# Optimization experiments

Measured on AMD Instinct MI355X. Metric: run time of the kernel, lower is better.

## Reference

```python
import math
import jax, jax.numpy as jnp
import numpy as np

N, C, H, W = 32, 128, 56, 56


def unfold3(x, axis, dil):
    """F.unfold with 3-tap kernel along `axis`, dilation `dil`, padding `dil`.
    Input (n,c,h,w) -> output (n,c,3,h,w); tap k takes offset (k-1)*dil."""
    pad_cfg = [(0, 0)] * 4
    pad_cfg[axis] = (dil, dil)
    xp = jnp.pad(x, pad_cfg)
    size = x.shape[axis]
    taps = [jax.lax.slice_in_dim(xp, k * dil, k * dil + size, axis=axis) for k in range(3)]
    return jnp.stack(taps, axis=2)


def setup_inputs() -> dict:
    key = jax.random.key(0)
    k0, k1, k2, k3, k4 = jax.random.split(key, 5)
    x = jax.random.normal(k0, (N, C, H, W), dtype=jnp.float32)
    # trunc_normal_(std=0.02) approximated by normal * 0.02
    p2 = jax.random.normal(k1, (1, 1, 3, 1, W), dtype=jnp.float32) * 0.02
    # 1x1 conv weight (out=C, in=3C), kaiming-ish scale
    p3 = jax.random.normal(k2, (C, 3 * C), dtype=jnp.float32) * (1.0 / math.sqrt(3 * C))
    p5 = jax.random.normal(k3, (1, 1, H, W), dtype=jnp.float32) * 0.02
    p10 = jax.random.normal(k4, (1, C, 3, H, W), dtype=jnp.float32) * 0.02
    return {"x": x, "p2": p2, "p3": p3, "p5": p5, "p10": p10}


def reference(x, p2, p3, p5, p10):
    n, c, h, w = x.shape
    # t_1: vertical 3-tap unfold, dilation 2 -> (n,c,3,h,w)
    t1 = unfold3(x, axis=2, dil=2)
    t2 = p2 * t1                                              # (n,c,3,h,w)
    # t_3: 1x1 conv over the c*3 channel view
    t3 = jnp.einsum('nkhw,ck->nchw', t1.reshape(n, c * 3, h, w), p3)
    # t_4: horizontal 3-tap unfold, dilation 1
    t4 = unfold3(t3, axis=3, dil=1)                           # (n,c,3,h,w)
    t5 = p5 * t3                                              # (n,c,h,w)
    # t_7/t_8: horizontal 3-tap unfold of x, dilation 2, softmax over taps
    t7 = unfold3(x, axis=3, dil=2)
    t8 = jax.nn.softmax(t7, axis=2)                           # (n,c,3,h,w)
    # t_9: bmm over spatial dim -> (n,c,c*3)
    t9 = jnp.einsum('ncx,ndx->ncd', x.reshape(n, c, h * w),
                    t4.reshape(n, c * 3, h * w)) / math.sqrt(h * w)
    t10 = p10 * t8                                            # (n,c,3,h,w)
    # t_11: memory-reinterpreting view: (n,1,c,h,w) - (n,3,c,h,w) -> back to (n,c,3,h,w)
    t11 = (t5[:, None] - t2.reshape(n, 3, c, h, w)).reshape(n, c, 3, h, w)
    t12 = t11 - t10                                           # (n,c,3,h,w)
    # t_13: bmm over c*3 -> (n,c,h*w)
    t13 = jnp.einsum('ncd,ndx->ncx', t9,
                     t12.reshape(n, c * 3, h * w)) / math.sqrt(c * 3)
    return t13.reshape(n, c, h, w)
```

## Files before the change

kernel.cpp:

```cpp
#include <hip/hip_runtime.h>
#include <stdint.h>

#define NB 32
#define C_ 128
#define H_ 56
#define W_ 56
#define HW 3136
#define KD 384

typedef __attribute__((ext_vector_type(8))) short bf16x8;
typedef __attribute__((ext_vector_type(4))) float f32x4;

__device__ inline uint16_t f2bf(float f) {
    uint32_t u = __float_as_uint(f);
    return (uint16_t)((u + 0x7FFFu + ((u >> 16) & 1u)) >> 16);
}
__device__ inline float bf2f(uint16_t b) {
    return __uint_as_float(((uint32_t)b) << 16);
}

__global__ __launch_bounds__(256) void p1_xtp(const float* __restrict__ x,
                                              uint16_t* __restrict__ xtp,
                                              uint16_t* __restrict__ xb) {
    __shared__ uint16_t lt[56][136];
    const int h = blockIdx.x, n = blockIdx.y, tid = threadIdx.x;
    const int c = tid >> 1, wh = tid & 1;
    const float* xr = &x[(((size_t)n * C_ + c) * H_ + h) * W_ + wh * 28];
    uint32_t pk[14];
#pragma unroll
    for (int q = 0; q < 7; ++q) {
        float4 v = *(const float4*)&xr[q * 4];
        int wb = wh * 28 + q * 4;
        uint16_t b0 = f2bf(v.x), b1 = f2bf(v.y), b2 = f2bf(v.z), b3 = f2bf(v.w);
        lt[wb + 0][c] = b0;
        lt[wb + 1][c] = b1;
        lt[wb + 2][c] = b2;
        lt[wb + 3][c] = b3;
        pk[q * 2]     = (uint32_t)b0 | ((uint32_t)b1 << 16);
        pk[q * 2 + 1] = (uint32_t)b2 | ((uint32_t)b3 << 16);
    }
    {
        uint16_t* xrow = &xb[(((size_t)n * C_ + c) * H_ + h) * 64 + wh * 28];
#pragma unroll
        for (int q = 0; q < 7; ++q)
            *(uint2*)&xrow[q * 4] = make_uint2(pk[q * 2], pk[q * 2 + 1]);
        if (wh == 1) {
            uint4 z = {0, 0, 0, 0};
            *(uint4*)&xrow[28] = z;
        }
    }
    __syncthreads();
    const int w = tid >> 2, qc = tid & 3;
    uint16_t* dst = &xtp[((((size_t)n * H_ + h) * 64 + w)) * C_ + qc * 32];
    if (w < 56) {
        const uint32_t* s = (const uint32_t*)&lt[w][qc * 32];
        uint4 a = *(const uint4*)(s);
        uint4 b = *(const uint4*)(s + 4);
        uint4 c4 = *(const uint4*)(s + 8);
        uint4 d4 = *(const uint4*)(s + 12);
        *(uint4*)dst = a;
        *(uint4*)(dst + 8) = b;
        *(uint4*)(dst + 16) = c4;
        *(uint4*)(dst + 24) = d4;
    } else {
        uint4 z = {0, 0, 0, 0};
        *(uint4*)dst = z;
        *(uint4*)(dst + 8) = z;
        *(uint4*)(dst + 16) = z;
        *(uint4*)(dst + 24) = z;
    }
}

__global__ __launch_bounds__(256) void p2_ap(const float* __restrict__ p3,
                                             uint16_t* __restrict__ ap) {
    int i = blockIdx.x * 256 + threadIdx.x;
    int c = i / KD, dp = i - c * KD;
    int tap = dp >> 7, c2 = dp & 127;
    ap[i] = f2bf(p3[c * KD + 3 * c2 + tap]);
}

__global__ __launch_bounds__(256) void k1(const uint16_t* __restrict__ xtp,
                                          const uint16_t* __restrict__ ap,
                                          uint16_t* __restrict__ t3b) {
    __shared__ uint16_t smem[3 * 32 * 128];
    const int bx = blockIdx.x, n = blockIdx.y, tid = threadIdx.x;
    const int h = bx >> 1, wbase = (bx & 1) << 5;
    const int lane = tid & 63, wid = tid >> 6;
    const int c15 = lane & 15, kq = lane >> 4;

    for (int t = tid; t < 1536; t += 256) {
        int tap = t >> 9, r = t & 511, w = r >> 4, qp = r & 15;
        int q = qp ^ (w & 7);
        int hh = h + 2 * (tap - 1);
        uint4 v = {0, 0, 0, 0};
        if ((unsigned)hh < (unsigned)H_)
            v = *(const uint4*)&xtp[((((size_t)n * H_ + hh) * 64 + wbase + w)) * C_ + q * 8];
        *(uint4*)&smem[tap * 4096 + w * 128 + qp * 8] = v;
    }
    __syncthreads();

    f32x4 acc[2][2] = {};
    for (int ks = 0; ks < 12; ++ks) {
        int tap = ks >> 2, kk = ks & 3;
        bf16x8 a[2], b[2];
#pragma unroll
        for (int m = 0; m < 2; ++m) {
            int c = wid * 32 + m * 16 + c15;
            a[m] = *(const bf16x8*)&ap[c * KD + ks * 32 + kq * 8];
        }
#pragma unroll
        for (int nt = 0; nt < 2; ++nt) {
            int w = nt * 16 + c15;
            int q = kk * 4 + kq;
            b[nt] = *(const bf16x8*)&smem[tap * 4096 + w * 128 + (q ^ (w & 7)) * 8];
        }
#pragma unroll
        for (int m = 0; m < 2; ++m)
#pragma unroll
            for (int nt = 0; nt < 2; ++nt)
                acc[m][nt] = __builtin_amdgcn_mfma_f32_16x16x32_bf16(a[m], b[nt], acc[m][nt], 0, 0, 0);
    }
    __syncthreads();

    uint16_t* lrow = smem;
#pragma unroll
    for (int m = 0; m < 2; ++m)
#pragma unroll
        for (int nt = 0; nt < 2; ++nt)
#pragma unroll
            for (int r = 0; r < 4; ++r) {
                int c = wid * 32 + m * 16 + kq * 4 + r;
                int wl = nt * 16 + c15;
                lrow[c * 40 + wl] = f2bf(acc[m][nt][r]);
            }
    __syncthreads();

    const uint32_t* lrowd = (const uint32_t*)smem;
    for (int t = tid; t < 512; t += 256) {
        int c = t >> 2, ch = t & 3;
        int m0 = c * 20 + ch * 4;
        uint4 o = make_uint4(lrowd[m0], lrowd[m0 + 1], lrowd[m0 + 2], lrowd[m0 + 3]);
        *(uint4*)&t3b[(((size_t)n * C_ + c) * H_ + h) * 64 + wbase + ch * 8] = o;
    }
}

__global__ __launch_bounds__(512) void k2(const uint16_t* __restrict__ xb,
                                          const uint16_t* __restrict__ t3b,
                                          uint16_t* __restrict__ part16) {
    __shared__ uint16_t xs[128 * 64];
    __shared__ uint16_t ts[128 * 64];
    const int bx = blockIdx.x;
    const int hc = bx / 3, tap = bx - hc * 3;
    const int n = blockIdx.y;
    const int tid = threadIdx.x, lane = tid & 63, wid = tid >> 6;
    const int wm = wid >> 2, wn = wid & 3;

    f32x4 acc[4][2] = {};
    for (int hr = 0; hr < 8; ++hr) {
        const int h = hc * 8 + hr;
        __syncthreads();
        for (int t = tid; t < 1024; t += 512) {
            int c = t >> 3, qp = t & 7, q = qp ^ (c & 7);
            uint4 v = *(const uint4*)&xb[(((size_t)n * C_ + c) * H_ + h) * 64 + q * 8];
            *(uint4*)&xs[c * 64 + qp * 8] = v;
        }
        for (int t = tid; t < 1024; t += 512) {
            int c2 = t >> 3, qp = t & 7, q = qp ^ (c2 & 7);
            const uint16_t* row = &t3b[(((size_t)n * C_ + c2) * H_ + h) * 64];
            uint4 v = *(const uint4*)&row[q * 8];
            uint4 o;
            if (tap == 1) {
                o = v;
            } else if (tap == 2) {
                uint32_t nx = (q < 7) ? *(const uint32_t*)&row[q * 8 + 8] : 0u;
                o.x = (v.y << 16) | (v.x >> 16);
                o.y = (v.z << 16) | (v.y >> 16);
                o.z = (v.w << 16) | (v.z >> 16);
                o.w = (nx << 16)  | (v.w >> 16);
            } else {
                uint32_t pv = (q > 0) ? *(const uint32_t*)&row[q * 8 - 2] : 0u;
                o.x = (v.x << 16) | (pv >> 16);
                o.y = (v.y << 16) | (v.x >> 16);
                o.z = (v.z << 16) | (v.y >> 16);
                o.w = (v.w << 16) | (v.z >> 16);
            }
            *(uint4*)&ts[c2 * 64 + qp * 8] = o;
        }
        __syncthreads();
#pragma unroll
        for (int ks = 0; ks < 2; ++ks) {
            bf16x8 a[4], b[2];
#pragma unroll
            for (int m = 0; m < 4; ++m) {
                int c = wm * 64 + m * 16 + (lane & 15);
                int q = ks * 4 + (lane >> 4);
                a[m] = *(const bf16x8*)&xs[c * 64 + (q ^ (c & 7)) * 8];
            }
#pragma unroll
            for (int nt = 0; nt < 2; ++nt) {
                int c2 = wn * 32 + nt * 16 + (lane & 15);
                int q = ks * 4 + (lane >> 4);
                b[nt] = *(const bf16x8*)&ts[c2 * 64 + (q ^ (c2 & 7)) * 8];
            }
#pragma unroll
            for (int m = 0; m < 4; ++m)
#pragma unroll
                for (int nt = 0; nt < 2; ++nt)
                    acc[m][nt] = __builtin_amdgcn_mfma_f32_16x16x32_bf16(a[m], b[nt], acc[m][nt], 0, 0, 0);
        }
    }
#pragma unroll
    for (int m = 0; m < 4; ++m)
#pragma unroll
        for (int nt = 0; nt < 2; ++nt)
#pragma unroll
            for (int r = 0; r < 4; ++r) {
                int c = wm * 64 + m * 16 + (lane >> 4) * 4 + r;
                int col = wn * 32 + nt * 16 + (lane & 15);
                part16[((((size_t)bx * NB + n) * C_ + c) << 7) + col] = f2bf(acc[m][nt][r]);
            }
}

__global__ __launch_bounds__(256) void kr(const uint16_t* __restrict__ part16,
                                          uint16_t* __restrict__ acat) {
    int idx = blockIdx.x * 256 + threadIdx.x;
    int fl = idx * 4;
    int nc = fl / KD, dp = fl - nc * KD;
    int tap = dp >> 7, c2 = dp & 127;
    float s0 = 0.f, s1 = 0.f, s2 = 0.f, s3 = 0.f;
#pragma unroll
    for (int hc = 0; hc < 7; ++hc) {
        uint2 v = *(const uint2*)&part16[((((size_t)(hc * 3 + tap)) * NB * C_ + nc) << 7) + c2];
        s0 += bf2f((uint16_t)(v.x & 0xffff));
        s1 += bf2f((uint16_t)(v.x >> 16));
        s2 += bf2f((uint16_t)(v.y & 0xffff));
        s3 += bf2f((uint16_t)(v.y >> 16));
    }
    const float sc = 1.f / 56.f;
    uint2 o;
    o.x = (uint32_t)f2bf(s0 * sc) | ((uint32_t)f2bf(s1 * sc) << 16);
    o.y = (uint32_t)f2bf(s2 * sc) | ((uint32_t)f2bf(s3 * sc) << 16);
    *(uint2*)&acat[(size_t)nc * 512 + dp] = o;
}

__global__ __launch_bounds__(256) void ka2(uint16_t* __restrict__ acat) {
    int t = blockIdx.x * 256 + threadIdx.x;
    int nc = t >> 3, m0 = (t & 7) * 16;
    uint16_t* row = &acat[(size_t)nc * 512];
#pragma unroll
    for (int mi = 0; mi < 16; ++mi) {
        int m = m0 + mi;
        float s = 0.f;
#pragma unroll
        for (int r = 0; r < 3; ++r) {
            int d = m + 128 * r;
            int q3 = d / 3;
            int dp = (d - q3 * 3) * 128 + q3;
            s += bf2f(row[dp]);
        }
        row[384 + m] = f2bf(s);
    }
}

__global__ __launch_bounds__(256) void kt(const float* __restrict__ p10,
                                          uint16_t* __restrict__ p10t) {
    const int h = blockIdx.x, tid = threadIdx.x;
    for (int idx = tid; idx < 3072; idx += 256) {
        int w = idx & 63, ch = idx >> 6;
        int dp0 = ch * 8;
        uint32_t pk[4];
#pragma unroll
        for (int j = 0; j < 8; ++j) {
            int dp = dp0 + j;
            int tap = dp >> 7, c2 = dp & 127;
            int dor = 3 * c2 + tap;
            float v = (w < W_) ? p10[(size_t)dor * HW + h * W_ + w] : 0.f;
            uint16_t bb = f2bf(v);
            if (j & 1) pk[j >> 1] |= ((uint32_t)bb) << 16;
            else       pk[j >> 1] = bb;
        }
        *(uint4*)&p10t[((size_t)h * 64 + w) * KD + dp0] = *(const uint4*)pk;
    }
}

__global__ __launch_bounds__(256, 4) void k3(const uint16_t* __restrict__ xtp,
                                             const uint16_t* __restrict__ t3b,
                                             const uint16_t* __restrict__ acat,
                                             const uint16_t* __restrict__ p10t,
                                             const float* __restrict__ p2,
                                             const float* __restrict__ p5,
                                             float* __restrict__ out) {
    __shared__ uint16_t tsm[32 * 512];
    const int bx = blockIdx.x, n = blockIdx.y, tid = threadIdx.x;
    const int h = bx >> 1, wbase = (bx & 1) << 5;
    const int lane = tid & 63, wid = tid >> 6;

    {
        const int w = tid & 31, seg = tid >> 5;
        const int wg = wbase + w;
        const int wsw = w & 7;
        float p2v[3];
#pragma unroll
        for (int tap = 0; tap < 3; ++tap)
            p2v[tap] = (wg < W_) ? p2[tap * W_ + wg] : 0.f;
        const size_t xrow = ((size_t)n * H_ + h) * 64;
        const int wgm2 = (wg >= 2) ? wg - 2 : 0;
        const int wgp2 = (wg + 2 < 64) ? wg + 2 : 63;

#pragma unroll
        for (int s = 0; s < 2; ++s) {
            const int c2b = (seg + s * 8) * 8;
            bf16x8 xh_v = *(const bf16x8*)&xtp[(xrow + wg) * C_ + c2b];
            bf16x8 xm_v = *(const bf16x8*)&xtp[(xrow + wgm2) * C_ + c2b];
            bf16x8 xp_v = *(const bf16x8*)&xtp[(xrow + wgp2) * C_ + c2b];
            float sm[3][8];
#pragma unroll
            for (int j = 0; j < 8; ++j) {
                float a1 = bf2f((uint16_t)xh_v[j]);
                float a0 = (wg >= 2) ? bf2f((uint16_t)xm_v[j]) : 0.f;
                float a2 = bf2f((uint16_t)xp_v[j]);
                float mx = fmaxf(a0, fmaxf(a1, a2));
                float e0 = __expf(a0 - mx), e1 = __expf(a1 - mx), e2 = __expf(a2 - mx);
                float rs = 1.f / (e0 + e1 + e2);
                sm[0][j] = e0 * rs; sm[1][j] = e1 * rs; sm[2][j] = e2 * rs;
            }
#pragma unroll
            for (int tap = 0; tap < 3; ++tap) {
                bf16x8 xhh;
                float p2e;
                if (tap == 1) { xhh = xh_v; p2e = p2v[1]; }
                else {
                    const int hh = h + 2 * (tap - 1);
                    const bool hok = (unsigned)hh < (unsigned)H_;
                    const int hhc = hok ? hh : h;
                    xhh = *(const bf16x8*)&xtp[(((size_t)n * H_ + hhc) * 64 + wg) * C_ + c2b];
                    p2e = hok ? p2v[tap] : 0.f;
                }
                bf16x8 pv = *(const bf16x8*)&p10t[((size_t)h * 64 + wg) * KD + tap * 128 + c2b];
                uint32_t pk[4];
#pragma unroll
                for (int j = 0; j < 8; ++j) {
                    float val = -(p2e * bf2f((uint16_t)xhh[j]) + bf2f((uint16_t)pv[j]) * sm[tap][j]);
                    uint16_t bb = f2bf(val);
                    if (j & 1) pk[j >> 1] |= ((uint32_t)bb) << 16;
                    else       pk[j >> 1] = bb;
                }
                int q = (tap * 128 + c2b) >> 3;
                *(uint4*)&tsm[w * 512 + ((q ^ wsw) << 3)] = *(const uint4*)pk;
            }
        }
    }

    {
        const int c2f = tid >> 1;
        const int whl = (tid & 1) << 4;
        const uint16_t* t3r = &t3b[(((size_t)n * C_ + c2f) * H_ + h) * 64 + wbase + whl];
        const int qf = 48 + (c2f >> 3);
        const int cf7 = c2f & 7;
#pragma unroll
        for (int g = 0; g < 2; ++g) {
            bf16x8 tv = *(const bf16x8*)&t3r[g * 8];
#pragma unroll
            for (int j = 0; j < 8; ++j) {
                int wl = whl + g * 8 + j;
                int wwg = wbase + wl;
                float p5v = (wwg < W_) ? p5[h * W_ + wwg] : 0.f;
                tsm[wl * 512 + ((qf ^ (wl & 7)) << 3) + cf7] = f2bf(p5v * bf2f((uint16_t)tv[j]));
            }
        }
    }
    __syncthreads();

    const int wm = wid;
    f32x4 acc[2][2] = {};
    for (int ks = 0; ks < 16; ++ks) {
        bf16x8 a[2], b[2];
#pragma unroll
        for (int m = 0; m < 2; ++m) {
            int c = wm * 32 + m * 16 + (lane & 15);
            a[m] = *(const bf16x8*)&acat[((size_t)n * C_ + c) * 512 + ks * 32 + (lane >> 4) * 8];
        }
#pragma unroll
        for (int nt = 0; nt < 2; ++nt) {
            int wl = nt * 16 + (lane & 15);
            int q = ks * 4 + (lane >> 4);
            b[nt] = *(const bf16x8*)&tsm[wl * 512 + ((q ^ (wl & 7)) << 3)];
        }
#pragma unroll
        for (int m = 0; m < 2; ++m)
#pragma unroll
            for (int nt = 0; nt < 2; ++nt)
                acc[m][nt] = __builtin_amdgcn_mfma_f32_16x16x32_bf16(a[m], b[nt], acc[m][nt], 0, 0, 0);
    }

    const float s = 0.05103103630798287f;
#pragma unroll
    for (int m = 0; m < 2; ++m)
#pragma unroll
        for (int nt = 0; nt < 2; ++nt) {
            int wwg = wbase + nt * 16 + (lane & 15);
            if (wwg < W_) {
                int c = wm * 32 + m * 16 + (lane >> 4) * 4;
                float* dst = &out[(((size_t)n * C_ + c) * H_ + h) * W_ + wwg];
#pragma unroll
                for (int r = 0; r < 4; ++r) dst[(size_t)r * HW] = acc[m][nt][r] * s;
            }
        }
}

extern "C" void kernel_launch(void* const* d_in, const int* in_sizes, int n_in,
                              void* d_out, int out_size, void* d_ws, size_t ws_size,
                              hipStream_t stream) {
    const float* x   = (const float*)d_in[0];
    const float* p2  = (const float*)d_in[1];
    const float* p3  = (const float*)d_in[2];
    const float* p5  = (const float*)d_in[3];
    const float* p10 = (const float*)d_in[4];
    float* out = (float*)d_out;

    uint8_t* w8 = (uint8_t*)d_ws;
    uint16_t* t3b    = (uint16_t*)(w8);
    uint16_t* ap     = (uint16_t*)(w8 + 29360128);
    uint16_t* xtp    = (uint16_t*)(w8 + 29458432);
    uint16_t* xb     = (uint16_t*)(w8 + 58818560);
    uint16_t* part16 = (uint16_t*)(w8 + 88178688);
    uint16_t* p10t   = (uint16_t*)(w8 + 88178688);
    uint16_t* acat   = (uint16_t*)(w8 + 110198784);

    p1_xtp<<<dim3(H_, NB), 256, 0, stream>>>(x, xtp, xb);
    p2_ap<<<dim3(192), 256, 0, stream>>>(p3, ap);
    k1<<<dim3(112, NB), 256, 0, stream>>>(xtp, ap, t3b);
    k2<<<dim3(21, NB), 512, 0, stream>>>(xb, t3b, part16);
    kr<<<dim3(1536), 256, 0, stream>>>(part16, acat);
    ka2<<<dim3(128), 256, 0, stream>>>(acat);
    kt<<<dim3(H_), 256, 0, stream>>>(p10, p10t);
    k3<<<dim3(112, NB), 256, 0, stream>>>(xtp, t3b, acat, p10t, p2, p5, out);
}
```

Measured before the change: 225.7 us.

## Split k2 blocks by output-channel quarter and build all three taps from one LDS tile

The t9 Gram kernel now splits blocks by h-chunk and a quarter of the c rows, instead of by h-chunk and tap. Each block loads the unshifted t3 row into LDS once and builds the three horizontal-shift B fragments in registers, running three MFMA chains per A fragment. This is meant to cut redundant t3 global loads and the per-tap shifting done during staging, at the cost of more blocks, each reloading t3 for its own c-quarter. The partial-sum layout changes to tap-major columns of width 384, and the reduction kernel is updated to match.

```diff
diff --git a/kernel.cpp b/kernel.cpp
--- a/kernel.cpp
+++ b/kernel.cpp
@@ -147,77 +147,73 @@
 __global__ __launch_bounds__(512) void k2(const uint16_t* __restrict__ xb,
                                           const uint16_t* __restrict__ t3b,
                                           uint16_t* __restrict__ part16) {
-    __shared__ uint16_t xs[128 * 64];
+    __shared__ uint16_t xs[32 * 64];
     __shared__ uint16_t ts[128 * 64];
     const int bx = blockIdx.x;
-    const int hc = bx / 3, tap = bx - hc * 3;
+    const int hc = bx >> 2, cq = bx & 3;
     const int n = blockIdx.y;
     const int tid = threadIdx.x, lane = tid & 63, wid = tid >> 6;
-    const int wm = wid >> 2, wn = wid & 3;
-
-    f32x4 acc[4][2] = {};
+    const int c15 = lane & 15, kq = lane >> 4;
+
+    f32x4 acc[2][3] = {};
     for (int hr = 0; hr < 8; ++hr) {
         const int h = hc * 8 + hr;
         __syncthreads();
-        for (int t = tid; t < 1024; t += 512) {
-            int c = t >> 3, qp = t & 7, q = qp ^ (c & 7);
-            uint4 v = *(const uint4*)&xb[(((size_t)n * C_ + c) * H_ + h) * 64 + q * 8];
-            *(uint4*)&xs[c * 64 + qp * 8] = v;
+        if (tid < 256) {
+            int cl = tid >> 3, qp = tid & 7, q = qp ^ (cl & 7);
+            uint4 v = *(const uint4*)&xb[(((size_t)n * C_ + cq * 32 + cl) * H_ + h) * 64 + q * 8];
+            *(uint4*)&xs[cl * 64 + qp * 8] = v;
         }
         for (int t = tid; t < 1024; t += 512) {
             int c2 = t >> 3, qp = t & 7, q = qp ^ (c2 & 7);
-            const uint16_t* row = &t3b[(((size_t)n * C_ + c2) * H_ + h) * 64];
-            uint4 v = *(const uint4*)&row[q * 8];
-            uint4 o;
-            if (tap == 1) {
-                o = v;
-            } else if (tap == 2) {
-                uint32_t nx = (q < 7) ? *(const uint32_t*)&row[q * 8 + 8] : 0u;
-                o.x = (v.y << 16) | (v.x >> 16);
-                o.y = (v.z << 16) | (v.y >> 16);
-                o.z = (v.w << 16) | (v.z >> 16);
-                o.w = (nx << 16)  | (v.w >> 16);
-            } else {
-                uint32_t pv = (q > 0) ? *(const uint32_t*)&row[q * 8 - 2] : 0u;
-                o.x = (v.x << 16) | (pv >> 16);
-                o.y = (v.y << 16) | (v.x >> 16);
-                o.z = (v.z << 16) | (v.y >> 16);
-                o.w = (v.w << 16) | (v.z >> 16);
-            }
-            *(uint4*)&ts[c2 * 64 + qp * 8] = o;
+            uint4 v = *(const uint4*)&t3b[(((size_t)n * C_ + c2) * H_ + h) * 64 + q * 8];
+            *(uint4*)&ts[c2 * 64 + qp * 8] = v;
         }
         __syncthreads();
 #pragma unroll
         for (int ks = 0; ks < 2; ++ks) {
-            bf16x8 a[4], b[2];
-#pragma unroll
-            for (int m = 0; m < 4; ++m) {
-                int c = wm * 64 + m * 16 + (lane & 15);
-                int q = ks * 4 + (lane >> 4);
-                a[m] = *(const bf16x8*)&xs[c * 64 + (q ^ (c & 7)) * 8];
-            }
-#pragma unroll
-            for (int nt = 0; nt < 2; ++nt) {
-                int c2 = wn * 32 + nt * 16 + (lane & 15);
-                int q = ks * 4 + (lane >> 4);
-                b[nt] = *(const bf16x8*)&ts[c2 * 64 + (q ^ (c2 & 7)) * 8];
-            }
-#pragma unroll
-            for (int m = 0; m < 4; ++m)
-#pragma unroll
-                for (int nt = 0; nt < 2; ++nt)
-                    acc[m][nt] = __builtin_amdgcn_mfma_f32_16x16x32_bf16(a[m], b[nt], acc[m][nt], 0, 0, 0);
-        }
-    }
-#pragma unroll
-    for (int m = 0; m < 4; ++m)
-#pragma unroll
-        for (int nt = 0; nt < 2; ++nt)
+            const int q = ks * 4 + kq;
+            bf16x8 a[2];
+#pragma unroll
+            for (int m = 0; m < 2; ++m) {
+                int cl = m * 16 + c15;
+                a[m] = *(const bf16x8*)&xs[cl * 64 + ((q ^ (cl & 7)) << 3)];
+            }
+            const int c2 = wid * 16 + c15;
+            const int base = c2 * 64;
+            const int s7 = c2 & 7;
+            uint4 v = *(const uint4*)&ts[base + ((q ^ s7) << 3)];
+            uint32_t pv = (q > 0) ? *(const uint32_t*)&ts[base + (((q - 1) ^ s7) << 3) + 6] : 0u;
+            uint32_t nx = (q < 7) ? *(const uint32_t*)&ts[base + (((q + 1) ^ s7) << 3)] : 0u;
+            uint4 b0, b2;
+            b0.x = (v.x << 16) | (pv >> 16);
+            b0.y = (v.y << 16) | (v.x >> 16);
+            b0.z = (v.z << 16) | (v.y >> 16);
+            b0.w = (v.w << 16) | (v.z >> 16);
+            b2.x = (v.y << 16) | (v.x >> 16);
+            b2.y = (v.z << 16) | (v.y >> 16);
+            b2.z = (v.w << 16) | (v.z >> 16);
+            b2.w = (nx << 16)  | (v.w >> 16);
+            bf16x8 bt0 = *(const bf16x8*)&b0;
+            bf16x8 bt1 = *(const bf16x8*)&v;
+            bf16x8 bt2 = *(const bf16x8*)&b2;
+#pragma unroll
+            for (int m = 0; m < 2; ++m) {
+                acc[m][0] = __builtin_amdgcn_mfma_f32_16x16x32_bf16(a[m], bt0, acc[m][0], 0, 0, 0);
+                acc[m][1] = __builtin_amdgcn_mfma_f32_16x16x32_bf16(a[m], bt1, acc[m][1], 0, 0, 0);
+                acc[m][2] = __builtin_amdgcn_mfma_f32_16x16x32_bf16(a[m], bt2, acc[m][2], 0, 0, 0);
+            }
+        }
+    }
+#pragma unroll
+    for (int m = 0; m < 2; ++m)
+#pragma unroll
+        for (int tap = 0; tap < 3; ++tap)
 #pragma unroll
             for (int r = 0; r < 4; ++r) {
-                int c = wm * 64 + m * 16 + (lane >> 4) * 4 + r;
-                int col = wn * 32 + nt * 16 + (lane & 15);
-                part16[((((size_t)bx * NB + n) * C_ + c) << 7) + col] = f2bf(acc[m][nt][r]);
+                int c = cq * 32 + m * 16 + kq * 4 + r;
+                int dp = tap * 128 + wid * 16 + c15;
+                part16[((size_t)(hc * NB + n) * C_ + c) * 384 + dp] = f2bf(acc[m][tap][r]);
             }
 }
 
@@ -226,11 +222,10 @@
     int idx = blockIdx.x * 256 + threadIdx.x;
     int fl = idx * 4;
     int nc = fl / KD, dp = fl - nc * KD;
-    int tap = dp >> 7, c2 = dp & 127;
     float s0 = 0.f, s1 = 0.f, s2 = 0.f, s3 = 0.f;
 #pragma unroll
     for (int hc = 0; hc < 7; ++hc) {
-        uint2 v = *(const uint2*)&part16[((((size_t)(hc * 3 + tap)) * NB * C_ + nc) << 7) + c2];
+        uint2 v = *(const uint2*)&part16[((size_t)hc * NB * C_ + nc) * 384 + dp];
         s0 += bf2f((uint16_t)(v.x & 0xffff));
         s1 += bf2f((uint16_t)(v.x >> 16));
         s2 += bf2f((uint16_t)(v.y & 0xffff));
@@ -430,7 +425,7 @@
     p1_xtp<<<dim3(H_, NB), 256, 0, stream>>>(x, xtp, xb);
     p2_ap<<<dim3(192), 256, 0, stream>>>(p3, ap);
     k1<<<dim3(112, NB), 256, 0, stream>>>(xtp, ap, t3b);
-    k2<<<dim3(21, NB), 512, 0, stream>>>(xb, t3b, part16);
+    k2<<<dim3(28, NB), 512, 0, stream>>>(xb, t3b, part16);
     kr<<<dim3(1536), 256, 0, stream>>>(part16, acat);
     ka2<<<dim3(128), 256, 0, stream>>>(acat);
     kt<<<dim3(H_), 256, 0, stream>>>(p10, p10t);
```

Result: no change. 227.4 us (+0.8%).
